# Kernel tuning notes

Hardware: AMD Instinct MI355X
Metric: run time of the kernel (lower is better)

Reference implementation:

```python
import jax, jax.numpy as jnp
import numpy as np

V, E, H, C, NC = 50000, 512, 512, 512, 2
B, T = 128, 512


def setup_inputs() -> dict:
    key = jax.random.key(0)
    ks = jax.random.split(key, 18)
    s = 0.05
    n = lambda k, shp: jax.random.normal(k, shp, dtype=jnp.float32) * s
    return {
        "tokens": jax.random.randint(ks[0], (B, T), 0, V, dtype=jnp.int32),
        "lengths": jax.random.randint(ks[1], (B,), T // 2, T + 1, dtype=jnp.int32),
        "emb": n(ks[2], (V, E)),
        "Wih_f": n(ks[3], (3 * H, E)), "Whh_f": n(ks[4], (3 * H, H)),
        "bih_f": n(ks[5], (3 * H,)), "bhh_f": n(ks[6], (3 * H,)),
        "Wih_b": n(ks[7], (3 * H, E)), "Whh_b": n(ks[8], (3 * H, H)),
        "bih_b": n(ks[9], (3 * H,)), "bhh_b": n(ks[10], (3 * H,)),
        "Wp": n(ks[11], (C, 2 * H)), "bp": n(ks[12], (C,)),
        "ctx": n(ks[13], (C,)),
        "Wl": n(ks[14], (NC, 2 * H)), "bl": n(ks[15], (NC,)),
    }


def _gru(x, mask, Wih, Whh, bih, bhh):
    """Unidirectional torch-style GRU. x:[B,T,E], mask:[B,T] -> [B,T,H].
    Hidden state is frozen on padded steps (pack_padded semantics)."""
    gi_all = jnp.swapaxes(x, 0, 1) @ Wih.T + bih  # [T,B,3H] input gates precomputed
    mT = jnp.swapaxes(mask, 0, 1)                 # [T,B]
    h0 = jnp.zeros((x.shape[0], Whh.shape[1]), x.dtype)

    def step(h, inp):
        gi, m = inp
        gh = h @ Whh.T + bhh
        ir, iz, i_n = jnp.split(gi, 3, axis=-1)
        hr, hz, h_n = jnp.split(gh, 3, axis=-1)
        r = jax.nn.sigmoid(ir + hr)
        z = jax.nn.sigmoid(iz + hz)
        nn_ = jnp.tanh(i_n + r * h_n)
        h_new = (1.0 - z) * nn_ + z * h
        h = jnp.where(m[:, None], h_new, h)
        return h, h

    _, out = jax.lax.scan(step, h0, (gi_all, mT))
    return jnp.swapaxes(out, 0, 1)


def _forward(tokens, lengths, emb, Wih_f, Whh_f, bih_f, bhh_f,
             Wih_b, Whh_b, bih_b, bhh_b, Wp, bp, ctx, Wl, bl):
    t_ar = jnp.arange(T)
    mask = t_ar[None, :] < lengths[:, None]          # [B,T] valid-token mask
    x = emb[tokens]                                   # [B,T,E]

    out_f = _gru(x, mask, Wih_f, Whh_f, bih_f, bhh_f)
    # reverse each sequence within its own length for the backward direction
    rev_idx = jnp.clip(lengths[:, None] - 1 - t_ar[None, :], 0, T - 1)  # [B,T]
    x_rev = jnp.take_along_axis(x, rev_idx[:, :, None], axis=1)
    out_b_rev = _gru(x_rev, mask, Wih_b, Whh_b, bih_b, bhh_b)
    out_b = jnp.take_along_axis(out_b_rev, rev_idx[:, :, None], axis=1)

    out = jnp.concatenate([out_f, out_b], axis=-1)    # [B,T,2H]
    out = out * mask[:, :, None].astype(out.dtype)    # zero pads (pad_packed_sequence)

    proj = jnp.tanh(out @ Wp.T + bp)                  # [B,T,C]
    scores = proj @ ctx                               # [B,T]
    scores = jnp.where(mask, scores, -jnp.inf)
    attn = jax.nn.softmax(scores, axis=1)             # masked softmax over valid words

    sent = jnp.einsum('bt,btd->bd', attn, out)        # attention pooling
    sent = jax.nn.selu(sent)                          # sentence_nonlinearity
    logits = sent @ Wl.T + bl                         # [B,NC]
    return logits, attn


def reference(tokens, lengths, emb, Wih_f, Whh_f, bih_f, bhh_f,
              Wih_b, Whh_b, bih_b, bhh_b, Wp, bp, ctx, Wl, bl):
    return _forward(tokens, lengths, emb, Wih_f, Whh_f, bih_f, bhh_f,
                    Wih_b, Whh_b, bih_b, bhh_b, Wp, bp, ctx, Wl, bl)
```

## Files before the change

kernel.cpp:

```cpp
#include <hip/hip_runtime.h>
#include <stdint.h>

#define B_  128
#define T_  512
#define H_  512
#define G3  1536

typedef __attribute__((ext_vector_type(8))) short bf16x8;
typedef __attribute__((ext_vector_type(4))) short bf16x4;
typedef __attribute__((ext_vector_type(4))) float f32x4;

#define MFMA16(a,b,c) __builtin_amdgcn_mfma_f32_16x16x32_bf16((a),(b),(c),0,0,0)

__device__ __forceinline__ unsigned short f2bf(float f) {
  union { float f; unsigned u; } v; v.f = f;
  unsigned r = v.u + 0x7FFFu + ((v.u >> 16) & 1u);
  return (unsigned short)(r >> 16);
}
__device__ __forceinline__ float bf2f(unsigned short u) {
  union { unsigned u; float f; } v; v.u = ((unsigned)u) << 16; return v.f;
}
__device__ __forceinline__ float sigm_f(float x) { return 1.f / (1.f + __expf(-x)); }
__device__ __forceinline__ float tanh_f(float x) { float e = __expf(2.f * x); return 1.f - 2.f / (e + 1.f); }

__launch_bounds__(256)
__global__ void k_cast(const float* __restrict__ Wih_f, const float* __restrict__ Wih_b,
                       const float* __restrict__ Whh_f, const float* __restrict__ Whh_b,
                       const float* __restrict__ Wp,
                       unsigned short* __restrict__ Wih, unsigned short* __restrict__ Whh,
                       unsigned short* __restrict__ Wpb, unsigned* __restrict__ flags) {
  int idx = blockIdx.x * 256 + threadIdx.x;
  if (idx < 65536) flags[idx] = 0;
  if (idx < 1572864) {
    float v = (idx < 786432) ? Wih_f[idx] : Wih_b[idx - 786432];
    Wih[idx] = f2bf(v);
  } else if (idx < 3145728) {
    int i2 = idx - 1572864;
    float v = (i2 < 786432) ? Whh_f[i2] : Whh_b[i2 - 786432];
    Whh[i2] = f2bf(v);
  } else if (idx < 3670016) {
    int i3 = idx - 3145728;
    Wpb[i3] = f2bf(Wp[i3]);
  }
}

__launch_bounds__(256)
__global__ void k_gather(const int* __restrict__ tokens, const float* __restrict__ emb,
                         unsigned short* __restrict__ xbf) {
  int row = blockIdx.x * 4 + (threadIdx.x >> 6);
  int lane = threadIdx.x & 63;
  int tok = tokens[row];
  const float4* src = (const float4*)(emb + (size_t)tok * 512);
  float4 v0 = src[lane * 2], v1 = src[lane * 2 + 1];
  bf16x8 pk;
  pk[0] = (short)f2bf(v0.x); pk[1] = (short)f2bf(v0.y);
  pk[2] = (short)f2bf(v0.z); pk[3] = (short)f2bf(v0.w);
  pk[4] = (short)f2bf(v1.x); pk[5] = (short)f2bf(v1.y);
  pk[6] = (short)f2bf(v1.z); pk[7] = (short)f2bf(v1.w);
  *(bf16x8*)&xbf[(size_t)row * 512 + lane * 8] = pk;
}

__launch_bounds__(256, 1)
__global__ void k_rec(const unsigned short* __restrict__ xbf,
                      const unsigned short* __restrict__ Wih,
                      const unsigned short* __restrict__ Whh,
                      const float* __restrict__ bih_f, const float* __restrict__ bih_b,
                      const float* __restrict__ bhh_f, const float* __restrict__ bhh_b,
                      const int* __restrict__ lengths,
                      unsigned short* __restrict__ hbuf,
                      unsigned short* __restrict__ outb,
                      unsigned* __restrict__ flags) {
  __shared__ bf16x8 wlds[6][16][64];
  __shared__ unsigned short htile[4][256];
  __shared__ unsigned short otile[4][256];
  __shared__ int role_s[2];

  unsigned* ctrl = flags + 511 * 128;

  if (threadIdx.x == 0) {
    unsigned xcd;
    asm volatile("s_getreg_b32 %0, hwreg(HW_REG_XCC_ID)" : "=s"(xcd));
    xcd &= 7u;
    unsigned slot = atomicAdd(&ctrl[xcd], 1u);
    unsigned gv;
    if (slot == 0u) {
      gv = atomicAdd(&ctrl[8], 1u) + 1u;
      __hip_atomic_store(&ctrl[16u + xcd], gv, __ATOMIC_RELAXED, __HIP_MEMORY_SCOPE_AGENT);
    } else {
      do {
        gv = __hip_atomic_load(&ctrl[16u + xcd], __ATOMIC_RELAXED, __HIP_MEMORY_SCOPE_AGENT);
      } while (gv == 0u);
    }
    int gq = (int)gv - 1;
    role_s[0] = (gq < 4 && slot < 32u) ? gq : -1;
    role_s[1] = (int)(slot & 31u);
  }
  __syncthreads();
  int g = role_s[0];
  if (g < 0) return;
  int j5 = role_s[1];

  int tid = threadIdx.x;
  int lane = tid & 63, w = tid >> 6;
  int quad = lane >> 4, l15 = lane & 15;
  int dir = g >> 1, mh = g & 1;
  int j0 = j5 << 4;
  int jg = j0 + l15;
  int rb = mh * 64 + w * 16;

  const unsigned short* wih_g = Wih + (size_t)dir * (G3 * H_);
  const unsigned short* whh_g = Whh + (size_t)dir * (G3 * H_);
  const float* bih = dir ? bih_b : bih_f;
  const float* bhh = dir ? bhh_b : bhh_f;
  float b_r  = bih[jg] + bhh[jg];
  float b_z  = bih[512 + jg] + bhh[512 + jg];
  float b_in = bih[1024 + jg];
  float b_hn = bhh[1024 + jg];

  for (int gi = w; gi < 6; gi += 4) {
    const unsigned short* base =
        (gi < 3 ? wih_g : whh_g) + (size_t)((gi % 3) * 512 + j0 + (lane & 15)) * 512;
    for (int s = 0; s < 16; ++s)
      wlds[gi][s][lane] = *(const bf16x8*)&base[s * 32 + (lane >> 4) * 8];
  }
  __syncthreads();

  int b0 = rb + l15;
  int L0 = lengths[b0];
  int Lg[4];
  #pragma unroll
  for (int r = 0; r < 4; ++r) Lg[r] = lengths[rb + 4 * quad + r];
  int bs = rb + (lane >> 2);
  int Ls = lengths[bs];
  int jp = lane & 3;

  unsigned short* hb = hbuf + (size_t)dir * (B_ * H_);
  float hreg[4] = {};

  bf16x8 ax[16];
  {
    int tx0 = dir ? (L0 - 1) : 0;
    const unsigned short* xr = xbf + ((size_t)b0 * T_ + tx0) * 512;
    #pragma unroll
    for (int s = 0; s < 16; ++s) ax[s] = *(const bf16x8*)&xr[s * 32 + quad * 8];
  }

  #pragma clang loop unroll(disable)
  for (int t = 0; t < T_; ++t) {
    const unsigned short* hc = hb + (size_t)(t & 1) * (2 * B_ * H_);
    unsigned short* hnx      = hb + (size_t)((t & 1) ^ 1) * (2 * B_ * H_);

    f32x4 acc_r = {0.f,0.f,0.f,0.f}, acc_z = {0.f,0.f,0.f,0.f};
    f32x4 acc_n = {0.f,0.f,0.f,0.f}, acc_h = {0.f,0.f,0.f,0.f};

    #pragma unroll
    for (int s = 0; s < 16; ++s) {
      acc_r = MFMA16(ax[s], wlds[0][s][lane], acc_r);
      acc_z = MFMA16(ax[s], wlds[1][s][lane], acc_z);
      acc_n = MFMA16(ax[s], wlds[2][s][lane], acc_n);
    }
    {
      int tn = (t + 1 < T_) ? (t + 1) : t;
      int tx1 = dir ? ((tn < L0) ? (L0 - 1 - tn) : 0) : tn;
      const unsigned short* xr1 = xbf + ((size_t)b0 * T_ + tx1) * 512;
      #pragma unroll
      for (int s = 0; s < 16; ++s) ax[s] = *(const bf16x8*)&xr1[s * 32 + quad * 8];
    }

    if (t > 0) {
      if (w == 0 && lane < 32) {
        const unsigned* fp = &flags[(size_t)(t - 1) * 128 + g * 32 + lane];
        int spin = 0;
        unsigned v;
        do {
          asm volatile("global_load_dword %0, %1, off sc0\n\ts_waitcnt vmcnt(0)"
                       : "=v"(v) : "v"(fp) : "memory");
          if (v != 0u) break;
          asm volatile("s_sleep 1" ::: "memory");
        } while (++spin < (1 << 15));
      }
      __syncthreads();
      const unsigned short* hr0 = hc + (size_t)b0 * H_;
      bf16x8 ah[16];
      #pragma unroll
      for (int s = 0; s < 16; ++s) {
        asm volatile("global_load_dwordx4 %0, %1, off sc0"
                     : "=v"(ah[s]) : "v"(hr0 + s * 32 + quad * 8) : "memory");
      }
      asm volatile("s_waitcnt vmcnt(0)" ::: "memory");
      __builtin_amdgcn_sched_barrier(0);
      #pragma unroll
      for (int s = 0; s < 16; ++s) {
        acc_r = MFMA16(ah[s], wlds[3][s][lane], acc_r);
        acc_z = MFMA16(ah[s], wlds[4][s][lane], acc_z);
        acc_h = MFMA16(ah[s], wlds[5][s][lane], acc_h);
      }
    }

    #pragma unroll
    for (int r = 0; r < 4; ++r) {
      int L = Lg[r];
      bool vld = t < L;
      float rr = sigm_f(acc_r[r] + b_r);
      float zz = sigm_f(acc_z[r] + b_z);
      float nn = tanh_f(acc_n[r] + b_in + rr * (acc_h[r] + b_hn));
      float hold = hreg[r];
      float hnew = vld ? ((1.f - zz) * nn + zz * hold) : hold;
      hreg[r] = hnew;
      unsigned short hbf = f2bf(hnew);
      htile[w][(4 * quad + r) * 16 + l15] = hbf;
      otile[w][(4 * quad + r) * 16 + l15] = vld ? hbf : (unsigned short)0;
    }
    asm volatile("s_waitcnt lgkmcnt(0)" ::: "memory");
    unsigned long long hv = *(const unsigned long long*)&htile[w][(lane >> 2) * 16 + jp * 4];
    unsigned long long ov = *(const unsigned long long*)&otile[w][(lane >> 2) * 16 + jp * 4];
    asm volatile("global_store_dwordx2 %0, %1, off sc0"
                 :: "v"(&hnx[(size_t)bs * H_ + j0 + jp * 4]), "v"(hv) : "memory");

    __syncthreads();
    if (tid == 0 && t < 511)
      asm volatile("global_store_dword %0, %1, off sc0"
                   :: "v"(&flags[(size_t)t * 128 + g * 32 + j5]), "v"(1u) : "memory");
    bool vs = t < Ls;
    int p = dir ? (vs ? (Ls - 1 - t) : t) : t;
    *(unsigned long long*)&outb[((size_t)bs * T_ + p) * 1024 + dir * 512 + j0 + jp * 4] = ov;
  }
}

__launch_bounds__(256)
__global__ void k_gemm2(const unsigned short* __restrict__ outbf,
                        const unsigned short* __restrict__ Wpb,
                        const float* __restrict__ bp, const float* __restrict__ ctx,
                        float* __restrict__ sc4) {
  __shared__ short smem[2 * 128 * 72];
  short* a_s = smem;
  short* b_s = smem + 128 * 72;
  int tid = threadIdx.x;
  int lane = tid & 63, w = tid >> 6;
  int quad = lane >> 4, l15 = lane & 15;
  int row0 = blockIdx.x * 128, col0 = blockIdx.y * 128;

  f32x4 acc[2][8];
  #pragma unroll
  for (int i = 0; i < 2; ++i)
    #pragma unroll
    for (int j = 0; j < 8; ++j) acc[i][j] = (f32x4){0.f, 0.f, 0.f, 0.f};

  for (int kt = 0; kt < 16; ++kt) {
    int k0 = kt * 64;
    __syncthreads();
    #pragma unroll
    for (int q = 0; q < 4; ++q) {
      int u = tid + 256 * q;
      int r = u >> 3, cu = u & 7;
      *(bf16x8*)&a_s[r * 72 + cu * 8] = *(const bf16x8*)&outbf[(size_t)(row0 + r) * 1024 + k0 + cu * 8];
      *(bf16x8*)&b_s[r * 72 + cu * 8] = *(const bf16x8*)&Wpb[(size_t)(col0 + r) * 1024 + k0 + cu * 8];
    }
    __syncthreads();
    #pragma unroll
    for (int kk = 0; kk < 2; ++kk) {
      int kb = kk * 32 + quad * 8;
      bf16x8 a0 = *(const bf16x8*)&a_s[(w * 32 + l15) * 72 + kb];
      bf16x8 a1 = *(const bf16x8*)&a_s[(w * 32 + 16 + l15) * 72 + kb];
      #pragma unroll
      for (int nt = 0; nt < 8; ++nt) {
        bf16x8 bb = *(const bf16x8*)&b_s[(nt * 16 + l15) * 72 + kb];
        acc[0][nt] = MFMA16(a0, bb, acc[0][nt]);
        acc[1][nt] = MFMA16(a1, bb, acc[1][nt]);
      }
    }
  }

  float rs[2][4] = {};
  #pragma unroll
  for (int mt = 0; mt < 2; ++mt) {
    #pragma unroll
    for (int nt = 0; nt < 8; ++nt) {
      int col = col0 + nt * 16 + l15;
      float bv = bp[col], cv = ctx[col];
      #pragma unroll
      for (int r = 0; r < 4; ++r) {
        float x = acc[mt][nt][r] + bv;
        rs[mt][r] += tanh_f(x) * cv;
      }
    }
  }
  #pragma unroll
  for (int mt = 0; mt < 2; ++mt) {
    #pragma unroll
    for (int r = 0; r < 4; ++r) {
      float v = rs[mt][r];
      v += __shfl_xor(v, 1); v += __shfl_xor(v, 2);
      v += __shfl_xor(v, 4); v += __shfl_xor(v, 8);
      if (l15 == 0)
        sc4[(size_t)blockIdx.y * 65536 + row0 + 32 * w + 16 * mt + 4 * quad + r] = v;
    }
  }
}

__launch_bounds__(64)
__global__ void k_softmax(const float* __restrict__ sc4, const int* __restrict__ lengths,
                          float* __restrict__ attn) {
  int b = blockIdx.x, lane = threadIdx.x;
  int L = lengths[b];
  float s[8]; float mx = -1e30f;
  #pragma unroll
  for (int i = 0; i < 8; ++i) {
    int t = lane + i * 64;
    int idx = b * T_ + t;
    float v = -1e30f;
    if (t < L)
      v = sc4[idx] + sc4[65536 + idx] + sc4[131072 + idx] + sc4[196608 + idx];
    s[i] = v;
    mx = fmaxf(mx, v);
  }
  #pragma unroll
  for (int o = 32; o; o >>= 1) mx = fmaxf(mx, __shfl_xor(mx, o));
  float sum = 0.f;
  #pragma unroll
  for (int i = 0; i < 8; ++i) {
    int t = lane + i * 64;
    s[i] = (t < L) ? __expf(s[i] - mx) : 0.f;
    sum += s[i];
  }
  #pragma unroll
  for (int o = 32; o; o >>= 1) sum += __shfl_xor(sum, o);
  float inv = 1.f / sum;
  #pragma unroll
  for (int i = 0; i < 8; ++i) attn[b * T_ + lane + i * 64] = s[i] * inv;
}

__launch_bounds__(256)
__global__ void k_final(const float* __restrict__ attn, const unsigned short* __restrict__ outb,
                        const int* __restrict__ lengths,
                        const float* __restrict__ Wl, const float* __restrict__ bl,
                        float* __restrict__ logits) {
  __shared__ float red[8];
  int b = blockIdx.x, tid = threadIdx.x;
  int L = lengths[b];
  float a0 = 0.f, a1 = 0.f, a2 = 0.f, a3 = 0.f;
  for (int t = 0; t < L; ++t) {
    float a = attn[b * T_ + t];
    const unsigned short* row = outb + ((size_t)b * T_ + t) * 1024 + tid * 4;
    bf16x4 v = *(const bf16x4*)row;
    a0 += a * bf2f((unsigned short)v[0]);
    a1 += a * bf2f((unsigned short)v[1]);
    a2 += a * bf2f((unsigned short)v[2]);
    a3 += a * bf2f((unsigned short)v[3]);
  }
  const float al = 1.6732632423543772f, sc = 1.0507009873554805f;
  float s0 = sc * (a0 > 0.f ? a0 : al * (__expf(a0) - 1.f));
  float s1 = sc * (a1 > 0.f ? a1 : al * (__expf(a1) - 1.f));
  float s2 = sc * (a2 > 0.f ? a2 : al * (__expf(a2) - 1.f));
  float s3 = sc * (a3 > 0.f ? a3 : al * (__expf(a3) - 1.f));
  int d = tid * 4;
  float p0 = s0 * Wl[d] + s1 * Wl[d + 1] + s2 * Wl[d + 2] + s3 * Wl[d + 3];
  float p1 = s0 * Wl[1024 + d] + s1 * Wl[1024 + d + 1] + s2 * Wl[1024 + d + 2] + s3 * Wl[1024 + d + 3];
  #pragma unroll
  for (int o = 32; o; o >>= 1) { p0 += __shfl_xor(p0, o); p1 += __shfl_xor(p1, o); }
  if ((tid & 63) == 0) { red[(tid >> 6) * 2] = p0; red[(tid >> 6) * 2 + 1] = p1; }
  __syncthreads();
  if (tid == 0) {
    logits[b * 2]     = red[0] + red[2] + red[4] + red[6] + bl[0];
    logits[b * 2 + 1] = red[1] + red[3] + red[5] + red[7] + bl[1];
  }
}

extern "C" void kernel_launch(void* const* d_in, const int* in_sizes, int n_in,
                              void* d_out, int out_size, void* d_ws, size_t ws_size,
                              hipStream_t stream) {
  const int*   tokens  = (const int*)d_in[0];
  const int*   lengths = (const int*)d_in[1];
  const float* emb     = (const float*)d_in[2];
  const float* Wih_f   = (const float*)d_in[3];
  const float* Whh_f   = (const float*)d_in[4];
  const float* bih_f   = (const float*)d_in[5];
  const float* bhh_f   = (const float*)d_in[6];
  const float* Wih_b   = (const float*)d_in[7];
  const float* Whh_b   = (const float*)d_in[8];
  const float* bih_b   = (const float*)d_in[9];
  const float* bhh_b   = (const float*)d_in[10];
  const float* Wp      = (const float*)d_in[11];
  const float* bp      = (const float*)d_in[12];
  const float* ctx     = (const float*)d_in[13];
  const float* Wl      = (const float*)d_in[14];
  const float* bl      = (const float*)d_in[15];
  float* out = (float*)d_out;

  char* ws = (char*)d_ws;
  unsigned short* Wih  = (unsigned short*)(ws + 0);
  unsigned short* Whh  = (unsigned short*)(ws + 3145728);
  unsigned short* Wpb  = (unsigned short*)(ws + 6291456);
  unsigned short* xbf  = (unsigned short*)(ws + 7340032);
  unsigned short* outb = (unsigned short*)(ws + 74448896);
  unsigned short* hbuf = (unsigned short*)(ws + 208666624);
  float* sc4           = (float*)(ws + 209190912);
  unsigned* flags      = (unsigned*)(ws + 210239488);

  k_cast<<<14336, 256, 0, stream>>>(Wih_f, Wih_b, Whh_f, Whh_b, Wp, Wih, Whh, Wpb, flags);
  k_gather<<<16384, 256, 0, stream>>>(tokens, emb, xbf);
  k_rec<<<1024, 256, 0, stream>>>(xbf, Wih, Whh, bih_f, bih_b, bhh_f, bhh_b,
                                  lengths, hbuf, outb, flags);
  dim3 g2(512, 4);
  k_gemm2<<<g2, 256, 0, stream>>>(outb, Wpb, bp, ctx, sc4);
  k_softmax<<<128, 64, 0, stream>>>(sc4, lengths, out + 256);
  k_final<<<128, 256, 0, stream>>>(out + 256, outb, lengths, Wl, bl, out);
}
```

Before: 3.329 ms.

## Precompute GRU input-gate projections with a separate MFMA GEMM before recurrence

Adds a batched bf16 MFMA GEMM that computes the input-gate projections x@Wih^T for all timesteps and both directions into a large fp32 workspace buffer, laid out per hidden tile. A new recurrent kernel then reads these precomputed gates, prefetching the next step's values, instead of computing the input projection inside the serial time loop. This takes the input GEMM off the latency-critical recurrence. In exchange it adds about 800MB of fp32 writes and reads, and it only runs when the workspace is large enough, falling back to the old kernel otherwise.

Measured after the change: 3.292 ms. No clear change (-1.1%).

```diff
diff --git a/kernel.cpp b/kernel.cpp
--- a/kernel.cpp
+++ b/kernel.cpp
@@ -58,6 +58,246 @@
   pk[4] = (short)f2bf(v1.x); pk[5] = (short)f2bf(v1.y);
   pk[6] = (short)f2bf(v1.z); pk[7] = (short)f2bf(v1.w);
   *(bf16x8*)&xbf[(size_t)row * 512 + lane * 8] = pk;
+}
+
+__launch_bounds__(256)
+__global__ void k_igemm(const unsigned short* __restrict__ xbf,
+                        const unsigned short* __restrict__ Wih,
+                        float* __restrict__ gi) {
+  __shared__ short smem[2 * 128 * 72];
+  short* a_s = smem;
+  short* b_s = smem + 128 * 72;
+  int tid = threadIdx.x;
+  int lane = tid & 63, w = tid >> 6;
+  int quad = lane >> 4, l15 = lane & 15;
+  int row0 = blockIdx.x * 128, col0 = blockIdx.y * 128;
+
+  f32x4 acc[2][8];
+  #pragma unroll
+  for (int i = 0; i < 2; ++i)
+    #pragma unroll
+    for (int j = 0; j < 8; ++j) acc[i][j] = (f32x4){0.f, 0.f, 0.f, 0.f};
+
+  for (int kt = 0; kt < 8; ++kt) {
+    int k0 = kt * 64;
+    __syncthreads();
+    #pragma unroll
+    for (int q = 0; q < 4; ++q) {
+      int u = tid + 256 * q;
+      int r = u >> 3, cu = u & 7;
+      *(bf16x8*)&a_s[r * 72 + cu * 8] = *(const bf16x8*)&xbf[(size_t)(row0 + r) * 512 + k0 + cu * 8];
+      *(bf16x8*)&b_s[r * 72 + cu * 8] = *(const bf16x8*)&Wih[(size_t)(col0 + r) * 512 + k0 + cu * 8];
+    }
+    __syncthreads();
+    #pragma unroll
+    for (int kk = 0; kk < 2; ++kk) {
+      int kb = kk * 32 + quad * 8;
+      bf16x8 a0 = *(const bf16x8*)&a_s[(w * 32 + l15) * 72 + kb];
+      bf16x8 a1 = *(const bf16x8*)&a_s[(w * 32 + 16 + l15) * 72 + kb];
+      #pragma unroll
+      for (int nt = 0; nt < 8; ++nt) {
+        bf16x8 bb = *(const bf16x8*)&b_s[(nt * 16 + l15) * 72 + kb];
+        acc[0][nt] = MFMA16(a0, bb, acc[0][nt]);
+        acc[1][nt] = MFMA16(a1, bb, acc[1][nt]);
+      }
+    }
+  }
+
+  int dir = col0 / 1536;
+  int c2b = col0 - dir * 1536;
+  int gate = c2b >> 9;
+  int jjb = c2b & 511;
+  size_t dbase = (size_t)dir * 65536ull * 1536ull;
+  #pragma unroll
+  for (int mt = 0; mt < 2; ++mt)
+    #pragma unroll
+    for (int nt = 0; nt < 8; ++nt) {
+      int j5 = (jjb >> 4) + nt;
+      #pragma unroll
+      for (int r = 0; r < 4; ++r) {
+        int row = row0 + 32 * w + 16 * mt + 4 * quad + r;
+        gi[dbase + (size_t)row * 1536 + j5 * 48 + gate * 16 + l15] = acc[mt][nt][r];
+      }
+    }
+}
+
+__launch_bounds__(256, 1)
+__global__ void k_rec2(const float* __restrict__ gi,
+                       const unsigned short* __restrict__ Whh,
+                       const float* __restrict__ bih_f, const float* __restrict__ bih_b,
+                       const float* __restrict__ bhh_f, const float* __restrict__ bhh_b,
+                       const int* __restrict__ lengths,
+                       unsigned short* __restrict__ hbuf,
+                       unsigned short* __restrict__ outb,
+                       unsigned* __restrict__ flags) {
+  __shared__ bf16x8 wlds[6][16][64];
+  __shared__ unsigned short htile[4][256];
+  __shared__ unsigned short otile[4][256];
+  __shared__ int role_s[2];
+
+  unsigned* ctrl = flags + 511 * 128;
+
+  if (threadIdx.x == 0) {
+    unsigned xcd;
+    asm volatile("s_getreg_b32 %0, hwreg(HW_REG_XCC_ID)" : "=s"(xcd));
+    xcd &= 7u;
+    unsigned slot = atomicAdd(&ctrl[xcd], 1u);
+    unsigned gv;
+    if (slot == 0u) {
+      gv = atomicAdd(&ctrl[8], 1u) + 1u;
+      __hip_atomic_store(&ctrl[16u + xcd], gv, __ATOMIC_RELAXED, __HIP_MEMORY_SCOPE_AGENT);
+    } else {
+      do {
+        gv = __hip_atomic_load(&ctrl[16u + xcd], __ATOMIC_RELAXED, __HIP_MEMORY_SCOPE_AGENT);
+      } while (gv == 0u);
+    }
+    int gq = (int)gv - 1;
+    role_s[0] = (gq < 4 && slot < 32u) ? gq : -1;
+    role_s[1] = (int)(slot & 31u);
+  }
+  __syncthreads();
+  int g = role_s[0];
+  if (g < 0) return;
+  int j5 = role_s[1];
+
+  int tid = threadIdx.x;
+  int lane = tid & 63, w = tid >> 6;
+  int quad = lane >> 4, l15 = lane & 15;
+  int dir = g >> 1, mh = g & 1;
+  int j0 = j5 << 4;
+  int jg = j0 + l15;
+  int rb = mh * 64 + w * 16;
+
+  const unsigned short* whh_g = Whh + (size_t)dir * (G3 * H_);
+  const float* bih = dir ? bih_b : bih_f;
+  const float* bhh = dir ? bhh_b : bhh_f;
+  float b_r  = bih[jg] + bhh[jg];
+  float b_z  = bih[512 + jg] + bhh[512 + jg];
+  float b_in = bih[1024 + jg];
+  float b_hn = bhh[1024 + jg];
+
+  for (int wt = w; wt < 3; wt += 4) {
+    const unsigned short* base =
+        whh_g + (size_t)(wt * 512 + j0 + (lane & 15)) * 512;
+    for (int s = 0; s < 16; ++s)
+      wlds[wt][s][lane] = *(const bf16x8*)&base[s * 32 + (lane >> 4) * 8];
+  }
+  __syncthreads();
+
+  int b0 = rb + l15;
+  int Lg[4];
+  #pragma unroll
+  for (int r = 0; r < 4; ++r) Lg[r] = lengths[rb + 4 * quad + r];
+  int bs = rb + (lane >> 2);
+  int Ls = lengths[bs];
+  int jp = lane & 3;
+
+  unsigned short* hb = hbuf + (size_t)dir * (B_ * H_);
+  float hreg[4] = {};
+
+  size_t dbase = (size_t)dir * 65536ull * 1536ull;
+  float gcur[12], gnxt[12];
+  #pragma unroll
+  for (int r = 0; r < 4; ++r) {
+    int tx = dir ? (Lg[r] - 1) : 0;
+    const float* gp = gi + dbase + ((size_t)(rb + 4 * quad + r) * T_ + tx) * 1536
+                      + j5 * 48 + l15;
+    gcur[3 * r + 0] = gp[0];
+    gcur[3 * r + 1] = gp[16];
+    gcur[3 * r + 2] = gp[32];
+  }
+
+  #pragma clang loop unroll(disable)
+  for (int t = 0; t < T_; ++t) {
+    const unsigned short* hc = hb + (size_t)(t & 1) * (2 * B_ * H_);
+    unsigned short* hnx      = hb + (size_t)((t & 1) ^ 1) * (2 * B_ * H_);
+
+    f32x4 acc_r = {0.f,0.f,0.f,0.f}, acc_z = {0.f,0.f,0.f,0.f};
+    f32x4 acc_h = {0.f,0.f,0.f,0.f};
+
+    if (t > 0) {
+      if (w == 0 && lane < 32) {
+        const unsigned* fp = &flags[(size_t)(t - 1) * 128 + g * 32 + lane];
+        int spin = 0;
+        unsigned v;
+        do {
+          asm volatile("global_load_dword %0, %1, off sc0\n\ts_waitcnt vmcnt(0)"
+                       : "=v"(v) : "v"(fp) : "memory");
+          if (v != 0u) break;
+          asm volatile("s_sleep 1" ::: "memory");
+        } while (++spin < (1 << 15));
+      }
+      __syncthreads();
+      const unsigned short* hr0 = hc + (size_t)b0 * H_;
+      bf16x8 ah[16];
+      #pragma unroll
+      for (int s = 0; s < 16; ++s) {
+        asm volatile("global_load_dwordx4 %0, %1, off sc0"
+                     : "=v"(ah[s]) : "v"(hr0 + s * 32 + quad * 8) : "memory");
+      }
+      asm volatile("s_waitcnt vmcnt(0)" ::: "memory");
+      __builtin_amdgcn_sched_barrier(0);
+      {
+        int tn = (t + 1 < T_) ? (t + 1) : t;
+        #pragma unroll
+        for (int r = 0; r < 4; ++r) {
+          int tx = dir ? ((tn < Lg[r]) ? (Lg[r] - 1 - tn) : 0) : tn;
+          const float* gp = gi + dbase + ((size_t)(rb + 4 * quad + r) * T_ + tx) * 1536
+                            + j5 * 48 + l15;
+          gnxt[3 * r + 0] = gp[0];
+          gnxt[3 * r + 1] = gp[16];
+          gnxt[3 * r + 2] = gp[32];
+        }
+      }
+      #pragma unroll
+      for (int s = 0; s < 16; ++s) {
+        acc_r = MFMA16(ah[s], wlds[0][s][lane], acc_r);
+        acc_z = MFMA16(ah[s], wlds[1][s][lane], acc_z);
+        acc_h = MFMA16(ah[s], wlds[2][s][lane], acc_h);
+      }
+    } else {
+      int tn = 1;
+      #pragma unroll
+      for (int r = 0; r < 4; ++r) {
+        int tx = dir ? ((tn < Lg[r]) ? (Lg[r] - 1 - tn) : 0) : tn;
+        const float* gp = gi + dbase + ((size_t)(rb + 4 * quad + r) * T_ + tx) * 1536
+                          + j5 * 48 + l15;
+        gnxt[3 * r + 0] = gp[0];
+        gnxt[3 * r + 1] = gp[16];
+        gnxt[3 * r + 2] = gp[32];
+      }
+    }
+
+    #pragma unroll
+    for (int r = 0; r < 4; ++r) {
+      int L = Lg[r];
+      bool vld = t < L;
+      float rr = sigm_f(acc_r[r] + gcur[3 * r + 0] + b_r);
+      float zz = sigm_f(acc_z[r] + gcur[3 * r + 1] + b_z);
+      float nn = tanh_f(gcur[3 * r + 2] + b_in + rr * (acc_h[r] + b_hn));
+      float hold = hreg[r];
+      float hnew = vld ? ((1.f - zz) * nn + zz * hold) : hold;
+      hreg[r] = hnew;
+      unsigned short hbf = f2bf(hnew);
+      htile[w][(4 * quad + r) * 16 + l15] = hbf;
+      otile[w][(4 * quad + r) * 16 + l15] = vld ? hbf : (unsigned short)0;
+    }
+    asm volatile("s_waitcnt lgkmcnt(0)" ::: "memory");
+    unsigned long long hv = *(const unsigned long long*)&htile[w][(lane >> 2) * 16 + jp * 4];
+    unsigned long long ov = *(const unsigned long long*)&otile[w][(lane >> 2) * 16 + jp * 4];
+    asm volatile("global_store_dwordx2 %0, %1, off sc0"
+                 :: "v"(&hnx[(size_t)bs * H_ + j0 + jp * 4]), "v"(hv) : "memory");
+    bool vs = t < Ls;
+    int p = dir ? (vs ? (Ls - 1 - t) : t) : t;
+    *(unsigned long long*)&outb[((size_t)bs * T_ + p) * 1024 + dir * 512 + j0 + jp * 4] = ov;
+
+    __syncthreads();
+    if (tid == 0 && t < 511)
+      asm volatile("global_store_dword %0, %1, off sc0"
+                   :: "v"(&flags[(size_t)t * 128 + g * 32 + j5]), "v"(1u) : "memory");
+    #pragma unroll
+    for (int i = 0; i < 12; ++i) gcur[i] = gnxt[i];
+  }
 }
 
 __launch_bounds__(256, 1)
@@ -396,11 +636,21 @@
   unsigned short* hbuf = (unsigned short*)(ws + 208666624);
   float* sc4           = (float*)(ws + 209190912);
   unsigned* flags      = (unsigned*)(ws + 210239488);
+  const size_t GI_OFF  = 210501632ull;
+  const size_t GI_SZ   = 805306368ull;
+  float* gi            = (float*)(ws + GI_OFF);
 
   k_cast<<<14336, 256, 0, stream>>>(Wih_f, Wih_b, Whh_f, Whh_b, Wp, Wih, Whh, Wpb, flags);
   k_gather<<<16384, 256, 0, stream>>>(tokens, emb, xbf);
-  k_rec<<<1024, 256, 0, stream>>>(xbf, Wih, Whh, bih_f, bih_b, bhh_f, bhh_b,
-                                  lengths, hbuf, outb, flags);
+  if (ws_size >= GI_OFF + GI_SZ) {
+    dim3 gg(512, 24);
+    k_igemm<<<gg, 256, 0, stream>>>(xbf, Wih, gi);
+    k_rec2<<<1024, 256, 0, stream>>>(gi, Whh, bih_f, bih_b, bhh_f, bhh_b,
+                                     lengths, hbuf, outb, flags);
+  } else {
+    k_rec<<<1024, 256, 0, stream>>>(xbf, Wih, Whh, bih_f, bih_b, bhh_f, bhh_b,
+                                    lengths, hbuf, outb, flags);
+  }
   dim3 g2(512, 4);
   k_gemm2<<<g2, 256, 0, stream>>>(outb, Wpb, bp, ctx, sc4);
   k_softmax<<<128, 64, 0, stream>>>(sc4, lengths, out + 256);
```
